# Kernel tuning notes

Hardware: AMD Instinct MI355X
Metric: run time of the kernel (lower is better)

Reference implementation:

```python
import jax, jax.numpy as jnp
import numpy as np
from math import log2, ceil

NUM_LEAVES = 128
KERNEL = 8
STRIDE = 8
PADDING = 0
LR = 0.3

LEAF_NUM = 2 ** ceil(log2(NUM_LEAVES))   # 128
DEPTH = int(log2(LEAF_NUM))              # 7
NUM_NODES = 2 * LEAF_NUM - 1             # 255


def _ancestor_table():
    # A[j-1, t-1] = global heap index of the ancestor of node j at tree level t,
    # or -1 if t exceeds j's own level. Nodes use heap indexing: children of i
    # are 2i+1, 2i+2 (matches the layer bookkeeping in the torch module).
    A = np.full((NUM_NODES - 1, DEPTH), -1, dtype=np.int32)
    for j in range(1, NUM_NODES):
        lvl = int(np.floor(np.log2(j + 1)))
        anc = j
        for t in range(lvl, 0, -1):
            A[j - 1, t - 1] = anc
            anc = (anc - 1) // 2
    return jnp.asarray(A)

_ANC = _ancestor_table()  # (NUM_NODES-1, DEPTH)


def img2patches(x):
    x = jnp.pad(x, PADDING)
    H, W = x.shape
    n0 = (H - KERNEL) // STRIDE + 1
    n1 = (W - KERNEL) // STRIDE + 1
    win = jnp.arange(KERNEL)
    rows = jnp.arange(n0)[:, None] * STRIDE + win[None, :]  # (n0, k)
    cols = jnp.arange(n1)[:, None] * STRIDE + win[None, :]  # (n1, k)
    p = x[rows[:, None, :, None], cols[None, :, None, :]]   # (n0, n1, k, k)
    return p.reshape(n0 * n1, KERNEL * KERNEL)


def setup_inputs() -> dict:
    key = jax.random.key(0)
    k1, k2 = jax.random.split(key)
    image = jax.random.uniform(k1, (2048, 2048), dtype=jnp.float32)
    nodes = jax.random.uniform(k2, (NUM_NODES, KERNEL * KERNEL), dtype=jnp.float32)
    return {"image": image, "nodes": nodes}


def reference(image, nodes):
    X = img2patches(image)                      # (P, k^2)
    P = X.shape[0]

    # --- hierarchical BMU descent (binary tree, DEPTH levels) ---
    cur = jnp.zeros((P,), dtype=jnp.int32)      # root
    bmu_levels = []
    for _ in range(DEPTH):
        c0 = 2 * cur + 1
        c1 = 2 * cur + 2
        # pnorm with p=2 in the source is (sum((a-b)^2))^2 -- monotone, kept faithful
        d0 = jnp.sum((nodes[c0] - X) ** 2, axis=-1) ** 2
        d1 = jnp.sum((nodes[c1] - X) ** 2, axis=-1) ** 2
        cur = jnp.where(d1 < d0, c1, c0)        # tie -> first (c0), like torch.min
        bmu_levels.append(cur)
    bmu_path = jnp.stack(bmu_levels, axis=1)    # (P, DEPTH), bmu at levels 1..DEPTH

    # --- layer_state for every non-root node: number of levels at which the
    # node's ancestor coincides with the BMU chain (== the torch concatenated
    # layer_state, columns ordered by global node index 1..NUM_NODES-1) ---
    state = jnp.sum(_ANC[None, :, :] == bmu_path[:, None, :], axis=-1)  # (P, N-1)

    lrates = LR * (2.0 ** jnp.arange(1, DEPTH + 2, dtype=jnp.float32)) / 2.0 ** (DEPTH + 1)
    lrs = lrates[state]                          # (P, N-1)

    # mean_p lrs[p,j] * (X[p,:] - nodes[1+j,:])
    #   = (lrs^T @ X)/P - mean_p(lrs)[:,None] * nodes[1:]
    upd = jnp.einsum('pj,pk->jk', lrs, X) / P - lrs.mean(axis=0)[:, None] * nodes[1:]
    new_nodes = nodes.at[1:].add(upd)

    return new_nodes, cur[:, None]               # updated codebook, leaf BMU per patch
```

## Files before the change

### kernel.cpp

```cpp
#include <hip/hip_runtime.h>

#define IMG_W 2048
#define NUM_NODES 255
#define DEPTH 7
#define NLEAF 128
#define NODE_STRIDE 68
#define S_STRIDE 68

__global__ __launch_bounds__(256) void phaseA(const float* __restrict__ img,
                                              const float* __restrict__ nodes,
                                              float* __restrict__ leaf_out,
                                              float* __restrict__ S_partial,
                                              unsigned* __restrict__ cnt_partial)
{
    __shared__ float nds[NUM_NODES * NODE_STRIDE];
    __shared__ float Sl[NLEAF * S_STRIDE];
    __shared__ unsigned cntl[NLEAF];

    const int t = threadIdx.x;
    const int b = blockIdx.x;

    for (int i = t; i < NLEAF * S_STRIDE; i += 256) Sl[i] = 0.0f;
    if (t < NLEAF) cntl[t] = 0;

    const float4* ng = (const float4*)nodes;
    for (int i = t; i < NUM_NODES * 16; i += 256) {
        int row = i >> 4, q = i & 15;
        float4 v = ng[i];
        *(float4*)&nds[row * NODE_STRIDE + q * 4] = v;
    }
    __syncthreads();

    const int p = b * 256 + t;
    const int r = p >> 8, c = p & 255;
    float4 xv[16];
    #pragma unroll
    for (int ki = 0; ki < 8; ++ki) {
        const float4* rowp = (const float4*)(img + (size_t)(r * 8 + ki) * IMG_W + c * 8);
        xv[ki * 2 + 0] = rowp[0];
        xv[ki * 2 + 1] = rowp[1];
    }

    int cur = 0;
    for (int lvl = 0; lvl < DEPTH; ++lvl) {
        const int c0 = 2 * cur + 1;
        const float* n0 = &nds[c0 * NODE_STRIDE];
        const float* n1 = n0 + NODE_STRIDE;
        float s0 = 0.f, s1 = 0.f;
        #pragma unroll
        for (int q = 0; q < 16; ++q) {
            float4 a  = *(const float4*)&n0[q * 4];
            float4 bb = *(const float4*)&n1[q * 4];
            float4 x  = xv[q];
            float d;
            d = a.x - x.x; s0 += d * d;  d = bb.x - x.x; s1 += d * d;
            d = a.y - x.y; s0 += d * d;  d = bb.y - x.y; s1 += d * d;
            d = a.z - x.z; s0 += d * d;  d = bb.z - x.z; s1 += d * d;
            d = a.w - x.w; s0 += d * d;  d = bb.w - x.w; s1 += d * d;
        }
        cur = (s1 < s0) ? (c0 + 1) : c0;
    }

    leaf_out[p] = (float)cur;
    const int L = cur - 127;

    #pragma unroll
    for (int q = 0; q < 16; ++q) {
        float* dst = &Sl[L * S_STRIDE + q * 4];
        float4 x = xv[q];
        atomicAdd(dst + 0, x.x);
        atomicAdd(dst + 1, x.y);
        atomicAdd(dst + 2, x.z);
        atomicAdd(dst + 3, x.w);
    }
    atomicAdd(&cntl[L], 1u);
    __syncthreads();

    float* Sp = S_partial + (size_t)b * (NLEAF * 64);
    for (int i = t; i < NLEAF * 16; i += 256) {
        int row = i >> 4, q = i & 15;
        float4 v = *(const float4*)&Sl[row * S_STRIDE + q * 4];
        *(float4*)&Sp[row * 64 + q * 4] = v;
    }
    if (t < NLEAF) cnt_partial[b * NLEAF + t] = cntl[t];
}

__global__ __launch_bounds__(256) void reduceS(const float* __restrict__ S_partial,
                                               const unsigned* __restrict__ cnt_partial,
                                               float* __restrict__ S,
                                               float* __restrict__ cnt)
{
    const int tid = blockIdx.x * 256 + threadIdx.x;
    float s = 0.f;
    for (int b = 0; b < 256; ++b) s += S_partial[(size_t)b * 8192 + tid];
    S[tid] = s;
    if (tid < NLEAF) {
        unsigned cc = 0;
        for (int b = 0; b < 256; ++b) cc += cnt_partial[b * NLEAF + tid];
        cnt[tid] = (float)cc;
    }
}

__global__ __launch_bounds__(64) void updateNodes(const float* __restrict__ nodes,
                                                  const float* __restrict__ S,
                                                  const float* __restrict__ cnt,
                                                  float* __restrict__ out)
{
    const int n = blockIdx.x;
    const int k = threadIdx.x;
    if (n == 0) { out[k] = nodes[k]; return; }

    const int pos = n + 1;
    const int Ln = 31 - __clz(pos);
    float su = 0.f, sc = 0.f;
    for (int L = 0; L < NLEAF; ++L) {
        const int a = (128 + L) >> (7 - Ln);
        const int x = pos ^ a;
        const int state = (x == 0) ? Ln : (Ln - (31 - __clz(x)) - 1);
        const float lr = 0.3f * ((float)(1 << state) * (1.0f / 128.0f));
        su += lr * S[L * 64 + k];
        sc += lr * cnt[L];
    }
    const float invP = 1.0f / 65536.0f;
    const float nd = nodes[n * 64 + k];
    out[n * 64 + k] = nd + su * invP - (sc * invP) * nd;
}

extern "C" void kernel_launch(void* const* d_in, const int* in_sizes, int n_in,
                              void* d_out, int out_size, void* d_ws, size_t ws_size,
                              hipStream_t stream)
{
    const float* img   = (const float*)d_in[0];
    const float* nodes = (const float*)d_in[1];

    float* out_nodes = (float*)d_out;
    float* out_leaf  = out_nodes + NUM_NODES * 64;

    float*    S_partial   = (float*)d_ws;
    unsigned* cnt_partial = (unsigned*)(S_partial + 256 * 8192);
    float*    S           = (float*)(cnt_partial + 256 * NLEAF);
    float*    cnt         = S + 8192;

    phaseA<<<256, 256, 0, stream>>>(img, nodes, out_leaf, S_partial, cnt_partial);
    reduceS<<<32, 256, 0, stream>>>(S_partial, cnt_partial, S, cnt);
    updateNodes<<<NUM_NODES, 64, 0, stream>>>(nodes, S, cnt, out_nodes);
}
```

Baseline: 123.0 us.

## Replace partial-sum reduction kernel with global atomics and staggered LDS accumulation

```diff
diff --git a/kernel.cpp b/kernel.cpp
--- a/kernel.cpp
+++ b/kernel.cpp
@@ -6,28 +6,36 @@
 #define NLEAF 128
 #define NODE_STRIDE 68
 #define S_STRIDE 68
+#define OVERLAY_FLOATS (256 * NODE_STRIDE)
+
+__global__ __launch_bounds__(256) void zeroS(float* __restrict__ S, unsigned* __restrict__ cnt)
+{
+    const int i = blockIdx.x * 256 + threadIdx.x;
+    if (i < NLEAF * 64) S[i] = 0.0f;
+    if (i < NLEAF) cnt[i] = 0u;
+}
 
 __global__ __launch_bounds__(256) void phaseA(const float* __restrict__ img,
                                               const float* __restrict__ nodes,
                                               float* __restrict__ leaf_out,
-                                              float* __restrict__ S_partial,
-                                              unsigned* __restrict__ cnt_partial)
+                                              float* __restrict__ S,
+                                              unsigned* __restrict__ cnt)
 {
-    __shared__ float nds[NUM_NODES * NODE_STRIDE];
-    __shared__ float Sl[NLEAF * S_STRIDE];
+    __shared__ float smem[OVERLAY_FLOATS + NLEAF * S_STRIDE];
     __shared__ unsigned cntl[NLEAF];
+    float* nds = smem;
+    float* Sl  = smem + OVERLAY_FLOATS;
 
     const int t = threadIdx.x;
     const int b = blockIdx.x;
 
     for (int i = t; i < NLEAF * S_STRIDE; i += 256) Sl[i] = 0.0f;
-    if (t < NLEAF) cntl[t] = 0;
+    if (t < NLEAF) cntl[t] = 0u;
 
     const float4* ng = (const float4*)nodes;
     for (int i = t; i < NUM_NODES * 16; i += 256) {
-        int row = i >> 4, q = i & 15;
-        float4 v = ng[i];
-        *(float4*)&nds[row * NODE_STRIDE + q * 4] = v;
+        const int row = i >> 4, q = i & 15;
+        *(float4*)&nds[row * NODE_STRIDE + q * 4] = ng[i];
     }
     __syncthreads();
 
@@ -42,6 +50,7 @@
     }
 
     int cur = 0;
+    #pragma unroll
     for (int lvl = 0; lvl < DEPTH; ++lvl) {
         const int c0 = 2 * cur + 1;
         const float* n0 = &nds[c0 * NODE_STRIDE];
@@ -49,9 +58,9 @@
         float s0 = 0.f, s1 = 0.f;
         #pragma unroll
         for (int q = 0; q < 16; ++q) {
-            float4 a  = *(const float4*)&n0[q * 4];
-            float4 bb = *(const float4*)&n1[q * 4];
-            float4 x  = xv[q];
+            const float4 a  = *(const float4*)&n0[q * 4];
+            const float4 bb = *(const float4*)&n1[q * 4];
+            const float4 x  = xv[q];
             float d;
             d = a.x - x.x; s0 += d * d;  d = bb.x - x.x; s1 += d * d;
             d = a.y - x.y; s0 += d * d;  d = bb.y - x.y; s1 += d * d;
@@ -64,62 +73,58 @@
     leaf_out[p] = (float)cur;
     const int L = cur - 127;
 
+    __syncthreads();
+
+    float* st = &nds[t * NODE_STRIDE];
     #pragma unroll
-    for (int q = 0; q < 16; ++q) {
-        float* dst = &Sl[L * S_STRIDE + q * 4];
-        float4 x = xv[q];
-        atomicAdd(dst + 0, x.x);
-        atomicAdd(dst + 1, x.y);
-        atomicAdd(dst + 2, x.z);
-        atomicAdd(dst + 3, x.w);
+    for (int q = 0; q < 16; ++q) *(float4*)&st[q * 4] = xv[q];
+
+    float* rowS = &Sl[L * S_STRIDE];
+    const int lane5 = 5 * (t & 63);
+    #pragma unroll 8
+    for (int s = 0; s < 64; ++s) {
+        const int e = (lane5 + s) & 63;
+        atomicAdd(&rowS[e], st[e]);
     }
     atomicAdd(&cntl[L], 1u);
     __syncthreads();
 
-    float* Sp = S_partial + (size_t)b * (NLEAF * 64);
-    for (int i = t; i < NLEAF * 16; i += 256) {
-        int row = i >> 4, q = i & 15;
-        float4 v = *(const float4*)&Sl[row * S_STRIDE + q * 4];
-        *(float4*)&Sp[row * 64 + q * 4] = v;
+    for (int i = t; i < NLEAF * 64; i += 256) {
+        const float v = Sl[(i >> 6) * S_STRIDE + (i & 63)];
+        if (v != 0.0f) atomicAdd(&S[i], v);
     }
-    if (t < NLEAF) cnt_partial[b * NLEAF + t] = cntl[t];
-}
-
-__global__ __launch_bounds__(256) void reduceS(const float* __restrict__ S_partial,
-                                               const unsigned* __restrict__ cnt_partial,
-                                               float* __restrict__ S,
-                                               float* __restrict__ cnt)
-{
-    const int tid = blockIdx.x * 256 + threadIdx.x;
-    float s = 0.f;
-    for (int b = 0; b < 256; ++b) s += S_partial[(size_t)b * 8192 + tid];
-    S[tid] = s;
-    if (tid < NLEAF) {
-        unsigned cc = 0;
-        for (int b = 0; b < 256; ++b) cc += cnt_partial[b * NLEAF + tid];
-        cnt[tid] = (float)cc;
-    }
+    if (t < NLEAF && cntl[t] != 0u) atomicAdd(&cnt[t], cntl[t]);
 }
 
 __global__ __launch_bounds__(64) void updateNodes(const float* __restrict__ nodes,
                                                   const float* __restrict__ S,
-                                                  const float* __restrict__ cnt,
+                                                  const unsigned* __restrict__ cnt,
                                                   float* __restrict__ out)
 {
     const int n = blockIdx.x;
     const int k = threadIdx.x;
     if (n == 0) { out[k] = nodes[k]; return; }
 
+    __shared__ float lrL[NLEAF];
+    __shared__ float cl[NLEAF];
+
     const int pos = n + 1;
     const int Ln = 31 - __clz(pos);
-    float su = 0.f, sc = 0.f;
-    for (int L = 0; L < NLEAF; ++L) {
+    for (int L = k; L < NLEAF; L += 64) {
         const int a = (128 + L) >> (7 - Ln);
         const int x = pos ^ a;
         const int state = (x == 0) ? Ln : (Ln - (31 - __clz(x)) - 1);
-        const float lr = 0.3f * ((float)(1 << state) * (1.0f / 128.0f));
-        su += lr * S[L * 64 + k];
-        sc += lr * cnt[L];
+        lrL[L] = 0.3f * ((float)(1 << state) * (1.0f / 128.0f));
+        cl[L]  = (float)cnt[L];
+    }
+    __syncthreads();
+
+    float su = 0.f, sc = 0.f;
+    #pragma unroll 8
+    for (int L = 0; L < NLEAF; ++L) {
+        const float lr = lrL[L];
+        su = fmaf(lr, S[L * 64 + k], su);
+        sc = fmaf(lr, cl[L], sc);
     }
     const float invP = 1.0f / 65536.0f;
     const float nd = nodes[n * 64 + k];
@@ -136,12 +141,10 @@
     float* out_nodes = (float*)d_out;
     float* out_leaf  = out_nodes + NUM_NODES * 64;
 
-    float*    S_partial   = (float*)d_ws;
-    unsigned* cnt_partial = (unsigned*)(S_partial + 256 * 8192);
-    float*    S           = (float*)(cnt_partial + 256 * NLEAF);
-    float*    cnt         = S + 8192;
+    float*    S   = (float*)d_ws;
+    unsigned* cnt = (unsigned*)(S + NLEAF * 64);
 
-    phaseA<<<256, 256, 0, stream>>>(img, nodes, out_leaf, S_partial, cnt_partial);
-    reduceS<<<32, 256, 0, stream>>>(S_partial, cnt_partial, S, cnt);
+    zeroS<<<33, 256, 0, stream>>>(S, cnt);
+    phaseA<<<256, 256, 0, stream>>>(img, nodes, out_leaf, S, cnt);
     updateNodes<<<NUM_NODES, 64, 0, stream>>>(nodes, S, cnt, out_nodes);
 }
```

Result: faster. 114.6 us (-6.8%).
